# Performance work log

Measured on AMD Instinct MI355X. Metric: run time of the kernel, lower is better.

## Reference

```python
import jax, jax.numpy as jnp
import numpy as np

# dims: n=batch, T=n_shifts, dX=16, dU=8, H=256 hidden, L=128 ldim, K=64 n_aux (L=2K)

def setup_inputs() -> dict:
    key = jax.random.key(0)
    ks = jax.random.split(key, 16)
    n, T, dX, dU, H, L, K = 64, 64, 16, 8, 256, 128, 64
    def lin(k, fan_in, shape):
        return (jax.random.uniform(k, shape, jnp.float32) * 2.0 - 1.0) / np.sqrt(fan_in)
    xs = jax.random.normal(ks[0], (n, T, dX), jnp.float32)
    us = jax.random.normal(ks[1], (n, T - 1, dU), jnp.float32)
    theta = jax.random.uniform(ks[2], (K,), jnp.float32) * (2.0 * np.pi)
    inp = {
        'xs': xs, 'us': us,
        # stacked x-aux encoders (K copies): BN affine, 3 linear layers (last no bias), output scale
        'x_gamma': jnp.ones((K, dX)), 'x_beta': jnp.zeros((K, dX)),
        'xW1': lin(ks[3], dX, (K, dX, H)), 'xb1': jnp.zeros((K, H)),
        'xW2': lin(ks[4], H, (K, H, H)), 'xb2': jnp.zeros((K, H)),
        'xW3': lin(ks[5], H, (K, H, L)), 'x_scale': jnp.ones((K, L)),
        # stacked u-aux encoders (K copies)
        'u_gamma': jnp.ones((K, dU)), 'u_beta': jnp.zeros((K, dU)),
        'uW1': lin(ks[6], dU, (K, dU, H)), 'ub1': jnp.zeros((K, H)),
        'uW2': lin(ks[7], H, (K, H, H)), 'ub2': jnp.zeros((K, H)),
        'uW3': lin(ks[8], H, (K, H, L)), 'u_scale': jnp.ones((K, L)),
        # Jordan-block complex eigenvalues (|lam| ~ 0.95)
        'reL': 0.95 * jnp.cos(theta), 'imL': 0.95 * jnp.sin(theta),
        # decoder C: Linear(ldim, dim, bias=False) -> weight [dX, L]
        'C_W': lin(ks[9], L, (dX, L)),
    }
    return inp


def _encoder(x, gamma, beta, W1, b1, W2, b2, W3, scale):
    # x: [M, D]; stacked params over K nets. BN stats (training mode) are per-feature over M,
    # identical across nets since the same x feeds every net.
    mu = x.mean(0)
    var = ((x - mu) ** 2).mean(0)
    xn = (x - mu) * jax.lax.rsqrt(var + 1e-5)          # [M, D]
    h = xn[None] * gamma[:, None, :] + beta[:, None, :]  # [K, M, D]
    h = jax.nn.leaky_relu(jnp.einsum('kmd,kdh->kmh', h, W1) + b1[:, None, :])
    h = jax.nn.leaky_relu(jnp.einsum('kmd,kdh->kmh', h, W2) + b2[:, None, :])
    h = jnp.einsum('kmd,kdh->kmh', h, W3)               # last layer: no bias
    return h * scale[:, None, :]                        # [K, M, L]


def reference(xs, us, x_gamma, x_beta, xW1, xb1, xW2, xb2, xW3, x_scale,
              u_gamma, u_beta, uW1, ub1, uW2, ub2, uW3, u_scale, reL, imL, C_W):
    n, T, dX = xs.shape
    K = reL.shape[0]
    L = 2 * K
    Tm1 = T - 1
    # phi1s: [n, T, K(net), K(pair), 2]
    phi = _encoder(xs.reshape(n * T, dX), x_gamma, x_beta, xW1, xb1, xW2, xb2, xW3, x_scale)
    phi1s = jnp.moveaxis(phi, 0, 1).reshape(n, T, K, K, 2)
    # ures = psi(u) - psi(0): [n, T-1, K, K, 2]
    uflat = us.reshape(n * Tm1, -1)
    psi_u = _encoder(uflat, u_gamma, u_beta, uW1, ub1, uW2, ub2, uW3, u_scale)
    psi_0 = _encoder(jnp.zeros_like(uflat), u_gamma, u_beta, uW1, ub1, uW2, ub2, uW3, u_scale)
    ures = jnp.moveaxis(psi_u - psi_0, 0, 1).reshape(n, Tm1, K, K, 2)
    # block-diagonal Koopman: per net j a 2x2 rotation-scale [[re, im], [-im, re]]
    R = jnp.stack([jnp.stack([reL, imL], -1), jnp.stack([-imL, reL], -1)], -2)  # [K, 2, 2]

    def step(p, u_t):
        p = jnp.einsum('bjkc,jcd->bjkd', p + u_t, R)
        return p, p

    _, preds = jax.lax.scan(step, phi1s[:, 0], jnp.moveaxis(ures, 0, 1))
    preds = jnp.moveaxis(preds, 0, 1)  # [n, T-1, K, K, 2]

    def phi2y(p):
        # sum over net axis (-3), flatten pair dims -> [.., L], decode with C
        return p.sum(-3).reshape(*p.shape[:-3], L) @ C_W.T

    y = phi2y(phi1s[:, 1:])
    y_pred = phi2y(preds)
    return y, y_pred
```

## Files before the change

kernel.cpp:

```cpp
#include <hip/hip_runtime.h>

typedef __bf16 bf16_t;
typedef __bf16 bf16x8 __attribute__((ext_vector_type(8)));
typedef __bf16 bf16x4 __attribute__((ext_vector_type(4)));
typedef float  f32x4  __attribute__((ext_vector_type(4)));

#define PHI_JS  (4096 * 128 + 64)
#define PSIU_JS (4032 * 128 + 64)

__global__ __launch_bounds__(256) void prep_all_kernel(
    const float* __restrict__ xW1, const float* __restrict__ xb1,
    const float* __restrict__ xg,  const float* __restrict__ xbeta,
    const float* __restrict__ uW1, const float* __restrict__ ub1,
    const float* __restrict__ ug,  const float* __restrict__ ubeta,
    const float* __restrict__ xW2, const float* __restrict__ uW2,
    const float* __restrict__ xW3, const float* __restrict__ uW3,
    const float* __restrict__ x_scale, const float* __restrict__ u_scale,
    const float* __restrict__ ub2,
    const float* __restrict__ xs, const float* __restrict__ us,
    bf16_t* __restrict__ xW1t, float* __restrict__ xb1p,
    bf16_t* __restrict__ uW1t, float* __restrict__ ub1p,
    bf16_t* __restrict__ xW2t, bf16_t* __restrict__ uW2t,
    bf16_t* __restrict__ xW3t, bf16_t* __restrict__ uW3t,
    float* __restrict__ psi0, float* __restrict__ part)
{
    const int t = blockIdx.x, tid = threadIdx.x;
    __shared__ float tile[32][33];
    __shared__ float h1[256], h2[256];

    if (t < 12288) {
        const float* in; bf16_t* outp; const float* scale = nullptr;
        int j, r0, c0, C;
        if (t < 8192) {
            C = 256;
            j = (t & 4095) >> 6;
            const int tl = t & 63; r0 = (tl >> 3) * 32; c0 = (tl & 7) * 32;
            if (t < 4096) { in = xW2; outp = xW2t; }
            else          { in = uW2; outp = uW2t; }
        } else {
            C = 128;
            const int l = t - 8192;
            j = (l & 2047) >> 5;
            const int tl = l & 31; r0 = (tl >> 2) * 32; c0 = (tl & 3) * 32;
            if (l < 2048) { in = xW3; outp = xW3t; scale = x_scale + j * 128; }
            else          { in = uW3; outp = uW3t; scale = u_scale + j * 128; }
        }
        const int R = 256;
        in   += (size_t)j * R * C;
        bf16_t* op = outp + (size_t)j * R * C;
        const int tx = tid & 31, ty = tid >> 5;
        #pragma unroll
        for (int i = 0; i < 4; i++)
            tile[ty + i * 8][tx] = in[(size_t)(r0 + ty + i * 8) * C + c0 + tx];
        __syncthreads();
        #pragma unroll
        for (int i = 0; i < 4; i++) {
            int c = c0 + ty + i * 8;
            float sc = scale ? scale[c] : 1.f;
            op[(size_t)c * R + r0 + tx] = (bf16_t)(tile[tx][ty + i * 8] * sc);
        }
    } else if (t < 12416) {
        const int bid = t - 12288, j = bid & 63, h = tid;
        const float *W1, *b1, *gamma, *beta; bf16_t* W1t; float* b1p; int D;
        if (bid < 64) { W1 = xW1; b1 = xb1; gamma = xg; beta = xbeta; W1t = xW1t; b1p = xb1p; D = 16; }
        else          { W1 = uW1; b1 = ub1; gamma = ug; beta = ubeta; W1t = uW1t; b1p = ub1p; D = 8; }
        float bacc = b1[j * 256 + h];
        bf16_t* orow = W1t + (size_t)(j * 256 + h) * 32;
        for (int d = 0; d < 32; d++) orow[d] = (bf16_t)0.f;
        for (int d = 0; d < D; d++) {
            float w = W1[((size_t)j * D + d) * 256 + h];
            orow[d] = (bf16_t)(gamma[j * D + d] * w);
            bacc += beta[j * D + d] * w;
        }
        b1p[j * 256 + h] = bacc;
    } else if (t < 12480) {
        const int j = t - 12416, h = tid;
        {
            float bacc = ub1[j * 256 + h];
            #pragma unroll
            for (int d = 0; d < 8; d++)
                bacc += ubeta[j * 8 + d] * uW1[((size_t)j * 8 + d) * 256 + h];
            h1[h] = fmaxf(bacc, 0.01f * bacc);
        }
        __syncthreads();
        {
            float acc = ub2[j * 256 + h];
            const float* w2 = uW2 + (size_t)j * 65536 + h;
            #pragma unroll 8
            for (int d = 0; d < 256; d++) acc += h1[d] * w2[d * 256];
            h2[h] = fmaxf(acc, 0.01f * acc);
        }
        __syncthreads();
        if (h < 128) {
            float acc = 0.f;
            const float* w3 = uW3 + (size_t)j * 32768 + h;
            #pragma unroll 8
            for (int d = 0; d < 256; d++) acc += h2[d] * w3[d * 128];
            psi0[j * 128 + h] = acc * u_scale[j * 128 + h];
        }
    } else {
        const int bid = t - 12480;
        const bool isx = bid < 64;
        const float* x = isx ? xs : us;
        const int D   = isx ? 16 : 8;
        const int lb  = isx ? bid : bid - 64;
        const int per = isx ? 1024 : 1008;
        const int start = lb * per;
        float a = 0.f, b = 0.f;
        for (int idx = start + tid; idx < start + per; idx += 256) {
            float v = x[idx];
            a += v; b += v * v;
        }
        float* s1 = h1; float* s2 = h2;
        s1[tid] = a; s2[tid] = b;
        __syncthreads();
        if (tid < D) {
            float sa = 0.f, sb = 0.f;
            for (int k = tid; k < 256; k += D) { sa += s1[k]; sb += s2[k]; }
            part[bid * 32 + tid]      = sa;
            part[bid * 32 + 16 + tid] = sb;
        }
    }
}

__global__ __launch_bounds__(512, 4) void fused_mlp_kernel(
    const float* __restrict__ xs, const float* __restrict__ us,
    const float* __restrict__ part,
    const bf16_t* __restrict__ xW1t, const float* __restrict__ xb1p,
    const bf16_t* __restrict__ xW2t, const float* __restrict__ xb2,
    const bf16_t* __restrict__ xW3t,
    const bf16_t* __restrict__ uW1t, const float* __restrict__ ub1p,
    const bf16_t* __restrict__ uW2t, const float* __restrict__ ub2,
    const bf16_t* __restrict__ uW3t,
    bf16_t* __restrict__ phi, bf16_t* __restrict__ psiu)
{
    const int bid  = blockIdx.x;
    const int xcd  = bid & 7;
    const int slot = bid >> 3;
    const int band = slot >> 6;
    const int t64  = slot & 63;
    const int j    = xcd * 8 + band;
    const bool is_x = t64 < 32;
    const int tile  = is_x ? t64 : (t64 - 32);

    const float*  In  = is_x ? xs   : us;
    const int     D   = is_x ? 16   : 8;
    const bf16_t* W1t = is_x ? xW1t : uW1t;
    const float*  b1p = is_x ? xb1p : ub1p;
    const bf16_t* W2t = is_x ? xW2t : uW2t;
    const float*  b2  = is_x ? xb2  : ub2;
    const bf16_t* W3t = is_x ? xW3t : uW3t;
    bf16_t* outp      = is_x ? phi  : psiu;
    const int M       = is_x ? 4096 : 4032;
    const size_t JS   = is_x ? (size_t)PHI_JS : (size_t)PSIU_JS;

    const int row0 = tile * 128;
    const int tid  = threadIdx.x;
    const int wave = tid >> 6;
    const int lane = tid & 63;
    const int quad = lane >> 4;
    const int l16  = lane & 15;
    const int lo2  = l16 & 3, hi2 = l16 >> 2;

    __shared__ __align__(16) bf16_t hs[128 * 256];
    __shared__ float stats_s[32];

    if (tid < 16) {
        if (is_x) {
            float sa = 0.f, sb = 0.f;
            #pragma unroll 8
            for (int b = 0; b < 64; b++) { sa += part[b * 32 + tid]; sb += part[b * 32 + 16 + tid]; }
            float mu = sa / 4096.f, var = sb / 4096.f - mu * mu;
            stats_s[tid] = mu; stats_s[16 + tid] = rsqrtf(var + 1e-5f);
        } else if (tid < 8) {
            float sa = 0.f, sb = 0.f;
            #pragma unroll 8
            for (int b = 64; b < 96; b++) { sa += part[b * 32 + tid]; sb += part[b * 32 + 16 + tid]; }
            float mu = sa / 4032.f, var = sb / 4032.f - mu * mu;
            stats_s[tid] = mu; stats_s[16 + tid] = rsqrtf(var + 1e-5f);
        }
    }
    __syncthreads();

    const f32x4 vzero = {0.f, 0.f, 0.f, 0.f};

    char* const hsB = (char*)hs;
    const char* const abase = hsB + l16 * 512 + ((quad ^ lo2) << 4);
    const int  wlow0 = (quad >> 1) ^ lo2;
    char* const wbase = hsB + l16 * 512 + ((wave ^ hi2) << 6) + ((quad & 1) << 3);

    {
        bf16x8 wfr[2];
        #pragma unroll
        for (int nbi = 0; nbi < 2; nbi++)
            wfr[nbi] = *reinterpret_cast<const bf16x8*>(
                W1t + (size_t)(j * 256 + wave * 32 + nbi * 16 + l16) * 32 + quad * 8);

        f32x4 acc[8][2];
        #pragma unroll
        for (int a = 0; a < 8; a++) { acc[a][0] = vzero; acc[a][1] = vzero; }

        const int c0 = quad * 8;
        #pragma unroll
        for (int mb = 0; mb < 8; mb++) {
            bf16x8 a;
            if (c0 < D) {
                int row = row0 + mb * 16 + l16;
                if (row > M - 1) row = M - 1;
                const float* xp = In + (size_t)row * D + c0;
                f32x4 v0 = *reinterpret_cast<const f32x4*>(xp);
                f32x4 v1 = *reinterpret_cast<const f32x4*>(xp + 4);
                #pragma unroll
                for (int e = 0; e < 4; e++) a[e]     = (bf16_t)((v0[e] - stats_s[c0 + e])     * stats_s[16 + c0 + e]);
                #pragma unroll
                for (int e = 0; e < 4; e++) a[4 + e] = (bf16_t)((v1[e] - stats_s[c0 + 4 + e]) * stats_s[16 + c0 + 4 + e]);
            } else {
                #pragma unroll
                for (int e = 0; e < 8; e++) a[e] = (bf16_t)0.f;
            }
            #pragma unroll
            for (int nbi = 0; nbi < 2; nbi++)
                acc[mb][nbi] = __builtin_amdgcn_mfma_f32_16x16x32_bf16(
                    wfr[nbi], a, acc[mb][nbi], 0, 0, 0);
        }

        #pragma unroll
        for (int nbi = 0; nbi < 2; nbi++) {
            const f32x4 bias = *reinterpret_cast<const f32x4*>(
                b1p + j * 256 + wave * 32 + nbi * 16 + quad * 4);
            char* wp = wbase + ((wlow0 ^ (nbi << 1)) << 4);
            #pragma unroll
            for (int mb = 0; mb < 8; mb++) {
                bf16x4 pk;
                #pragma unroll
                for (int r = 0; r < 4; r++) {
                    float v = acc[mb][nbi][r] + bias[r];
                    v = fmaxf(v, 0.01f * v);
                    pk[r] = (bf16_t)v;
                }
                *reinterpret_cast<bf16x4*>(wp + mb * 8192) = pk;
            }
        }
    }
    __syncthreads();

    {
        f32x4 acc[8][2];
        #pragma unroll
        for (int a = 0; a < 8; a++) { acc[a][0] = vzero; acc[a][1] = vzero; }

        const bf16_t* w2base = W2t + ((size_t)j * 256 + wave * 32 + l16) * 256 + quad * 8;

        bf16x8 wr[3][2];
        #pragma unroll
        for (int d = 0; d < 3; d++)
            #pragma unroll
            for (int nbi = 0; nbi < 2; nbi++)
                wr[d][nbi] = *reinterpret_cast<const bf16x8*>(w2base + nbi * 4096 + d * 32);

        #pragma unroll
        for (int kk = 0; kk < 8; kk++) {
            const int c = kk % 3;
            const char* ap = abase + ((kk ^ hi2) << 6);
            bf16x8 av0[4];
            #pragma unroll
            for (int mb = 0; mb < 4; mb++)
                av0[mb] = *reinterpret_cast<const bf16x8*>(ap + mb * 8192);
            #pragma unroll
            for (int nbi = 0; nbi < 2; nbi++)
                #pragma unroll
                for (int mb = 0; mb < 4; mb++)
                    acc[mb][nbi] = __builtin_amdgcn_mfma_f32_16x16x32_bf16(
                        wr[c][nbi], av0[mb], acc[mb][nbi], 0, 0, 0);
            bf16x8 av1[4];
            #pragma unroll
            for (int mb = 0; mb < 4; mb++)
                av1[mb] = *reinterpret_cast<const bf16x8*>(ap + (mb + 4) * 8192);
            #pragma unroll
            for (int nbi = 0; nbi < 2; nbi++)
                #pragma unroll
                for (int mb = 4; mb < 8; mb++)
                    acc[mb][nbi] = __builtin_amdgcn_mfma_f32_16x16x32_bf16(
                        wr[c][nbi], av1[mb - 4], acc[mb][nbi], 0, 0, 0);
            if (kk < 5) {
                #pragma unroll
                for (int nbi = 0; nbi < 2; nbi++)
                    wr[c][nbi] = *reinterpret_cast<const bf16x8*>(
                        w2base + nbi * 4096 + (kk + 3) * 32);
            }
        }
        __syncthreads();
        #pragma unroll
        for (int nbi = 0; nbi < 2; nbi++) {
            const f32x4 bias = *reinterpret_cast<const f32x4*>(
                b2 + j * 256 + wave * 32 + nbi * 16 + quad * 4);
            char* wp = wbase + ((wlow0 ^ (nbi << 1)) << 4);
            #pragma unroll
            for (int mb = 0; mb < 8; mb++) {
                bf16x4 pk;
                #pragma unroll
                for (int r = 0; r < 4; r++) {
                    float v = acc[mb][nbi][r] + bias[r];
                    v = fmaxf(v, 0.01f * v);
                    pk[r] = (bf16_t)v;
                }
                *reinterpret_cast<bf16x4*>(wp + mb * 8192) = pk;
            }
        }
    }
    __syncthreads();

    {
        f32x4 acc[8];
        #pragma unroll
        for (int a = 0; a < 8; a++) acc[a] = vzero;

        const bf16_t* w3base = W3t + ((size_t)j * 128 + wave * 16 + l16) * 256 + quad * 8;

        bf16x8 wr[3];
        #pragma unroll
        for (int d = 0; d < 3; d++)
            wr[d] = *reinterpret_cast<const bf16x8*>(w3base + d * 32);

        #pragma unroll
        for (int kk = 0; kk < 8; kk++) {
            const int c = kk % 3;
            const char* ap = abase + ((kk ^ hi2) << 6);
            bf16x8 av0[4];
            #pragma unroll
            for (int mb = 0; mb < 4; mb++)
                av0[mb] = *reinterpret_cast<const bf16x8*>(ap + mb * 8192);
            #pragma unroll
            for (int mb = 0; mb < 4; mb++)
                acc[mb] = __builtin_amdgcn_mfma_f32_16x16x32_bf16(
                    wr[c], av0[mb], acc[mb], 0, 0, 0);
            bf16x8 av1[4];
            #pragma unroll
            for (int mb = 0; mb < 4; mb++)
                av1[mb] = *reinterpret_cast<const bf16x8*>(ap + (mb + 4) * 8192);
            #pragma unroll
            for (int mb = 4; mb < 8; mb++)
                acc[mb] = __builtin_amdgcn_mfma_f32_16x16x32_bf16(
                    wr[c], av1[mb - 4], acc[mb], 0, 0, 0);
            if (kk < 5)
                wr[c] = *reinterpret_cast<const bf16x8*>(w3base + (kk + 3) * 32);
        }
        __syncthreads();
        {
            const int sp3 = (wave * 2 + (quad >> 1)) ^ l16;
            char* w3p = hsB + l16 * 256 + sp3 * 16 + ((quad & 1) << 3);
            #pragma unroll
            for (int mb = 0; mb < 8; mb++) {
                bf16x4 pk;
                #pragma unroll
                for (int r = 0; r < 4; r++) pk[r] = (bf16_t)acc[mb][r];
                *reinterpret_cast<bf16x4*>(w3p + mb * 4096) = pk;
            }
        }
    }
    __syncthreads();
    #pragma unroll
    for (int p = 0; p < 4; p++) {
        const int rr = p * 32 + (tid >> 4);
        const int s  = tid & 15;
        if (row0 + rr < M) {
            bf16x8 v = *reinterpret_cast<const bf16x8*>(hs + rr * 128 + (s ^ (rr & 15)) * 8);
            *reinterpret_cast<bf16x8*>(outp + (size_t)j * JS + (size_t)(row0 + rr) * 128 + s * 8) = v;
        }
    }
}

__global__ __launch_bounds__(256) void scan_kernel(
    const bf16_t* __restrict__ phi, const bf16_t* __restrict__ psiu,
    const float* __restrict__ psi0, const float* __restrict__ reL,
    const float* __restrict__ imL, float* __restrict__ scratchP,
    float* __restrict__ scratchY) {
    const int b = blockIdx.x >> 3, jg = blockIdx.x & 7;
    const int tid = threadIdx.x;
    const int wave = tid >> 6, lane = tid & 63;
    __shared__ float redP[2][4][128];
    __shared__ float redY[2][4][128];

    const int j0 = jg * 8 + wave * 2;
    float sx0, sy0, sx1, sy1;
    float p0x0, p0y0, p0x1, p0y1, lre0, lim0, lre1, lim1;
    {
        unsigned v0 = *reinterpret_cast<const unsigned*>(
            phi + (size_t)j0 * PHI_JS + (size_t)(b * 64) * 128 + lane * 2);
        unsigned v1 = *reinterpret_cast<const unsigned*>(
            phi + (size_t)(j0 + 1) * PHI_JS + (size_t)(b * 64) * 128 + lane * 2);
        sx0 = __uint_as_float(v0 << 16); sy0 = __uint_as_float(v0 & 0xFFFF0000u);
        sx1 = __uint_as_float(v1 << 16); sy1 = __uint_as_float(v1 & 0xFFFF0000u);
        float2 p0 = *reinterpret_cast<const float2*>(psi0 + j0 * 128 + lane * 2);
        float2 p1 = *reinterpret_cast<const float2*>(psi0 + (j0 + 1) * 128 + lane * 2);
        p0x0 = p0.x; p0y0 = p0.y; p0x1 = p1.x; p0y1 = p1.y;
        lre0 = reL[j0]; lim0 = imL[j0]; lre1 = reL[j0 + 1]; lim1 = imL[j0 + 1];
    }
    const bf16_t* up0 = psiu + (size_t)j0 * PSIU_JS + (size_t)(b * 63) * 128 + lane * 2;
    const bf16_t* up1 = psiu + (size_t)(j0 + 1) * PSIU_JS + (size_t)(b * 63) * 128 + lane * 2;
    const bf16_t* pp0 = phi + (size_t)j0 * PHI_JS + (size_t)(b * 64 + 1) * 128 + lane * 2;
    const bf16_t* pp1 = phi + (size_t)(j0 + 1) * PHI_JS + (size_t)(b * 64 + 1) * 128 + lane * 2;
    unsigned cur0 = *reinterpret_cast<const unsigned*>(up0);
    unsigned cur1 = *reinterpret_cast<const unsigned*>(up1);
    unsigned curp0 = *reinterpret_cast<const unsigned*>(pp0);
    unsigned curp1 = *reinterpret_cast<const unsigned*>(pp1);
    float* outP = scratchP + (size_t)blockIdx.x * 63 * 128;
    float* outY = scratchY + (size_t)blockIdx.x * 63 * 128;

    for (int t = 0; t < 63; t++) {
        unsigned nx0 = 0, nx1 = 0, np0 = 0, np1 = 0;
        if (t < 62) {
            nx0 = *reinterpret_cast<const unsigned*>(up0 + (t + 1) * 128);
            nx1 = *reinterpret_cast<const unsigned*>(up1 + (t + 1) * 128);
            np0 = *reinterpret_cast<const unsigned*>(pp0 + (t + 1) * 128);
            np1 = *reinterpret_cast<const unsigned*>(pp1 + (t + 1) * 128);
        }
        float px = sx0 + (__uint_as_float(cur0 << 16) - p0x0);
        float py = sy0 + (__uint_as_float(cur0 & 0xFFFF0000u) - p0y0);
        sx0 = px * lre0 - py * lim0;
        sy0 = px * lim0 + py * lre0;
        px = sx1 + (__uint_as_float(cur1 << 16) - p0x1);
        py = sy1 + (__uint_as_float(cur1 & 0xFFFF0000u) - p0y1);
        sx1 = px * lre1 - py * lim1;
        sy1 = px * lim1 + py * lre1;
        float yx = __uint_as_float(curp0 << 16) + __uint_as_float(curp1 << 16);
        float yy = __uint_as_float(curp0 & 0xFFFF0000u) + __uint_as_float(curp1 & 0xFFFF0000u);
        const int db = t & 1;
        redP[db][wave][lane * 2]     = sx0 + sx1;
        redP[db][wave][lane * 2 + 1] = sy0 + sy1;
        redY[db][wave][lane * 2]     = yx;
        redY[db][wave][lane * 2 + 1] = yy;
        __syncthreads();
        if (tid < 128)
            outP[t * 128 + tid] = redP[db][0][tid] + redP[db][1][tid]
                                + redP[db][2][tid] + redP[db][3][tid];
        else {
            const int tl = tid - 128;
            outY[t * 128 + tl] = redY[db][0][tl] + redY[db][1][tl]
                               + redY[db][2][tl] + redY[db][3][tl];
        }
        cur0 = nx0; cur1 = nx1; curp0 = np0; curp1 = np1;
    }
}

__global__ __launch_bounds__(256) void decode_kernel(
    const float* __restrict__ scratchP, const float* __restrict__ scratchY,
    const float* __restrict__ C_W,
    float* __restrict__ y, float* __restrict__ ypred) {
    const int tg = threadIdx.x >> 6;
    const int l  = threadIdx.x & 63;
    const int t  = blockIdx.x * 4 + tg;
    const int b  = blockIdx.y;
    __shared__ float SP[4][128];
    __shared__ float SY[4][128];
    if (t < 63) {
        float s0 = 0.f, s1 = 0.f, u0 = 0.f, u1 = 0.f;
        #pragma unroll
        for (int jg = 0; jg < 8; jg++) {
            const size_t base = ((size_t)(b * 8 + jg) * 63 + t) * 128 + l * 2;
            float2 vp = *reinterpret_cast<const float2*>(scratchP + base);
            float2 vy = *reinterpret_cast<const float2*>(scratchY + base);
            s0 += vp.x; s1 += vp.y;
            u0 += vy.x; u1 += vy.y;
        }
        SP[tg][l * 2] = s0; SP[tg][l * 2 + 1] = s1;
        SY[tg][l * 2] = u0; SY[tg][l * 2 + 1] = u1;
        const int o = l >> 2, q = l & 3;
        float accP = 0.f, accY = 0.f;
        #pragma unroll
        for (int i = 0; i < 32; i++) {
            const float c = C_W[o * 128 + q * 32 + i];
            accP += SP[tg][q * 32 + i] * c;
            accY += SY[tg][q * 32 + i] * c;
        }
        accP += __shfl_xor(accP, 2, 4);
        accP += __shfl_xor(accP, 1, 4);
        accY += __shfl_xor(accY, 2, 4);
        accY += __shfl_xor(accY, 1, 4);
        if (q == 0) {
            ypred[(b * 63 + t) * 16 + o] = accP;
            y[(b * 63 + t) * 16 + o]     = accY;
        }
    }
}

extern "C" void kernel_launch(void* const* d_in, const int* in_sizes, int n_in,
                              void* d_out, int out_size, void* d_ws, size_t ws_size,
                              hipStream_t stream) {
    const float* xs      = (const float*)d_in[0];
    const float* us      = (const float*)d_in[1];
    const float* x_gamma = (const float*)d_in[2];
    const float* x_beta  = (const float*)d_in[3];
    const float* xW1     = (const float*)d_in[4];
    const float* xb1     = (const float*)d_in[5];
    const float* xW2     = (const float*)d_in[6];
    const float* xb2     = (const float*)d_in[7];
    const float* xW3     = (const float*)d_in[8];
    const float* x_scale = (const float*)d_in[9];
    const float* u_gamma = (const float*)d_in[10];
    const float* u_beta  = (const float*)d_in[11];
    const float* uW1     = (const float*)d_in[12];
    const float* ub1     = (const float*)d_in[13];
    const float* uW2     = (const float*)d_in[14];
    const float* ub2     = (const float*)d_in[15];
    const float* uW3     = (const float*)d_in[16];
    const float* u_scale = (const float*)d_in[17];
    const float* reL     = (const float*)d_in[18];
    const float* imL     = (const float*)d_in[19];
    const float* C_W     = (const float*)d_in[20];

    char* ws = (char*)d_ws;
    size_t off = 0;
    auto alloc = [&](size_t bytes) -> char* {
        char* p = ws + off;
        off += (bytes + 255) & ~(size_t)255;
        return p;
    };
    float*  part = (float*)alloc(96 * 32 * 4);
    bf16_t* xW1t = (bf16_t*)alloc((size_t)64 * 256 * 32 * 2);
    float*  xb1p = (float*) alloc((size_t)64 * 256 * 4);
    bf16_t* xW2t = (bf16_t*)alloc((size_t)64 * 256 * 256 * 2);
    bf16_t* xW3t = (bf16_t*)alloc((size_t)64 * 128 * 256 * 2);
    bf16_t* uW1t = (bf16_t*)alloc((size_t)64 * 256 * 32 * 2);
    float*  ub1p = (float*) alloc((size_t)64 * 256 * 4);
    bf16_t* uW2t = (bf16_t*)alloc((size_t)64 * 256 * 256 * 2);
    bf16_t* uW3t = (bf16_t*)alloc((size_t)64 * 128 * 256 * 2);
    float*  psi0 = (float*) alloc((size_t)64 * 128 * 4);
    bf16_t* phi  = (bf16_t*)alloc((size_t)64 * PHI_JS  * 2);
    bf16_t* psiu = (bf16_t*)alloc((size_t)64 * PSIU_JS * 2);
    float*  scrP = (float*) alloc((size_t)512 * 63 * 128 * 4);
    float*  scrY = (float*) alloc((size_t)512 * 63 * 128 * 4);

    float* y_out     = (float*)d_out;
    float* ypred_out = y_out + 64 * 63 * 16;

    prep_all_kernel<<<12576, 256, 0, stream>>>(
        xW1, xb1, x_gamma, x_beta, uW1, ub1, u_gamma, u_beta,
        xW2, uW2, xW3, uW3, x_scale, u_scale, ub2, xs, us,
        xW1t, xb1p, uW1t, ub1p, xW2t, uW2t, xW3t, uW3t, psi0, part);
    fused_mlp_kernel<<<4096, 512, 0, stream>>>(
        xs, us, part,
        xW1t, xb1p, xW2t, xb2, xW3t, uW1t, ub1p, uW2t, ub2, uW3t, phi, psiu);
    scan_kernel<<<512, 256, 0, stream>>>(phi, psiu, psi0, reL, imL, scrP, scrY);
    decode_kernel<<<dim3(16, 64), 256, 0, stream>>>(scrP, scrY, C_W, y_out, ypred_out);
}
```

Baseline: 355.7 us.

## Fuse decode into scan via atomics and move psi0 MLP into fused kernel

```diff
diff --git a/kernel.cpp b/kernel.cpp
--- a/kernel.cpp
+++ b/kernel.cpp
@@ -16,13 +16,12 @@
     const float* __restrict__ xW2, const float* __restrict__ uW2,
     const float* __restrict__ xW3, const float* __restrict__ uW3,
     const float* __restrict__ x_scale, const float* __restrict__ u_scale,
-    const float* __restrict__ ub2,
     const float* __restrict__ xs, const float* __restrict__ us,
     bf16_t* __restrict__ xW1t, float* __restrict__ xb1p,
     bf16_t* __restrict__ uW1t, float* __restrict__ ub1p,
     bf16_t* __restrict__ xW2t, bf16_t* __restrict__ uW2t,
     bf16_t* __restrict__ xW3t, bf16_t* __restrict__ uW3t,
-    float* __restrict__ psi0, float* __restrict__ part)
+    float* __restrict__ part, float* __restrict__ zout)
 {
     const int t = blockIdx.x, tid = threadIdx.x;
     __shared__ float tile[32][33];
@@ -73,33 +72,8 @@
             bacc += beta[j * D + d] * w;
         }
         b1p[j * 256 + h] = bacc;
-    } else if (t < 12480) {
-        const int j = t - 12416, h = tid;
-        {
-            float bacc = ub1[j * 256 + h];
-            #pragma unroll
-            for (int d = 0; d < 8; d++)
-                bacc += ubeta[j * 8 + d] * uW1[((size_t)j * 8 + d) * 256 + h];
-            h1[h] = fmaxf(bacc, 0.01f * bacc);
-        }
-        __syncthreads();
-        {
-            float acc = ub2[j * 256 + h];
-            const float* w2 = uW2 + (size_t)j * 65536 + h;
-            #pragma unroll 8
-            for (int d = 0; d < 256; d++) acc += h1[d] * w2[d * 256];
-            h2[h] = fmaxf(acc, 0.01f * acc);
-        }
-        __syncthreads();
-        if (h < 128) {
-            float acc = 0.f;
-            const float* w3 = uW3 + (size_t)j * 32768 + h;
-            #pragma unroll 8
-            for (int d = 0; d < 256; d++) acc += h2[d] * w3[d * 128];
-            psi0[j * 128 + h] = acc * u_scale[j * 128 + h];
-        }
-    } else {
-        const int bid = t - 12480;
+    } else if (t < 12512) {
+        const int bid = t - 12416;
         const bool isx = bid < 64;
         const float* x = isx ? xs : us;
         const int D   = isx ? 16 : 8;
@@ -120,6 +94,10 @@
             part[bid * 32 + tid]      = sa;
             part[bid * 32 + 16 + tid] = sb;
         }
+    } else {
+        const int g = (t - 12512) * 256 + tid;
+        for (int i = g; i < 2 * 64 * 63 * 16; i += 64 * 256)
+            zout[i] = 0.f;
     }
 }
 
@@ -132,9 +110,62 @@
     const bf16_t* __restrict__ uW1t, const float* __restrict__ ub1p,
     const bf16_t* __restrict__ uW2t, const float* __restrict__ ub2,
     const bf16_t* __restrict__ uW3t,
+    const float* __restrict__ uW1r, const float* __restrict__ ub1r,
+    const float* __restrict__ ubetar, const float* __restrict__ uW2r,
+    const float* __restrict__ uW3r, const float* __restrict__ u_scaler,
+    float* __restrict__ psi0_out,
     bf16_t* __restrict__ phi, bf16_t* __restrict__ psiu)
 {
     const int bid  = blockIdx.x;
+    const int tid  = threadIdx.x;
+
+    __shared__ __align__(16) bf16_t hs[128 * 256];
+    __shared__ float stats_s[32];
+
+    if (bid >= 4096) {
+        const int j = bid - 4096;
+        float* fb  = (float*)hs;
+        float* h1  = fb;
+        float* h2  = fb + 256;
+        float* tmp = fb + 512;
+        const int h = tid & 255, half = tid >> 8;
+        if (half == 0) {
+            float bacc = ub1r[j * 256 + h];
+            #pragma unroll
+            for (int d = 0; d < 8; d++)
+                bacc += ubetar[j * 8 + d] * uW1r[((size_t)j * 8 + d) * 256 + h];
+            h1[h] = fmaxf(bacc, 0.01f * bacc);
+        }
+        __syncthreads();
+        {
+            float acc = (half == 0) ? ub2[j * 256 + h] : 0.f;
+            const float* w2 = uW2r + (size_t)j * 65536 + (size_t)half * 128 * 256 + h;
+            #pragma unroll 16
+            for (int d = 0; d < 128; d++) acc += h1[half * 128 + d] * w2[(size_t)d * 256];
+            tmp[tid] = acc;
+        }
+        __syncthreads();
+        if (half == 0) {
+            float v = tmp[h] + tmp[h + 256];
+            h2[h] = fmaxf(v, 0.01f * v);
+        }
+        __syncthreads();
+        {
+            const int h3 = tid & 127, qd = tid >> 7;
+            float acc = 0.f;
+            const float* w3 = uW3r + (size_t)j * 32768 + (size_t)qd * 64 * 128 + h3;
+            #pragma unroll 16
+            for (int d = 0; d < 64; d++) acc += h2[qd * 64 + d] * w3[(size_t)d * 128];
+            tmp[tid] = acc;
+        }
+        __syncthreads();
+        if (tid < 128)
+            psi0_out[j * 128 + tid] =
+                (tmp[tid] + tmp[tid + 128] + tmp[tid + 256] + tmp[tid + 384])
+                * u_scaler[j * 128 + tid];
+        return;
+    }
+
     const int xcd  = bid & 7;
     const int slot = bid >> 3;
     const int band = slot >> 6;
@@ -155,15 +186,11 @@
     const size_t JS   = is_x ? (size_t)PHI_JS : (size_t)PSIU_JS;
 
     const int row0 = tile * 128;
-    const int tid  = threadIdx.x;
     const int wave = tid >> 6;
     const int lane = tid & 63;
     const int quad = lane >> 4;
     const int l16  = lane & 15;
     const int lo2  = l16 & 3, hi2 = l16 >> 2;
-
-    __shared__ __align__(16) bf16_t hs[128 * 256];
-    __shared__ float stats_s[32];
 
     if (tid < 16) {
         if (is_x) {
@@ -373,13 +400,17 @@
 __global__ __launch_bounds__(256) void scan_kernel(
     const bf16_t* __restrict__ phi, const bf16_t* __restrict__ psiu,
     const float* __restrict__ psi0, const float* __restrict__ reL,
-    const float* __restrict__ imL, float* __restrict__ scratchP,
-    float* __restrict__ scratchY) {
+    const float* __restrict__ imL, const float* __restrict__ C_W,
+    float* __restrict__ y, float* __restrict__ ypred) {
     const int b = blockIdx.x >> 3, jg = blockIdx.x & 7;
     const int tid = threadIdx.x;
     const int wave = tid >> 6, lane = tid & 63;
     __shared__ float redP[2][4][128];
     __shared__ float redY[2][4][128];
+    __shared__ float SP[128], SY[128];
+    __shared__ float Cs[2048];
+    #pragma unroll
+    for (int i = 0; i < 8; i++) Cs[tid + i * 256] = C_W[tid + i * 256];
 
     const int j0 = jg * 8 + wave * 2;
     float sx0, sy0, sx1, sy1;
@@ -404,8 +435,8 @@
     unsigned cur1 = *reinterpret_cast<const unsigned*>(up1);
     unsigned curp0 = *reinterpret_cast<const unsigned*>(pp0);
     unsigned curp1 = *reinterpret_cast<const unsigned*>(pp1);
-    float* outP = scratchP + (size_t)blockIdx.x * 63 * 128;
-    float* outY = scratchY + (size_t)blockIdx.x * 63 * 128;
+
+    const int oo = (tid & 127) >> 3, qq = tid & 7;
 
     for (int t = 0; t < 63; t++) {
         unsigned nx0 = 0, nx1 = 0, np0 = 0, np1 = 0;
@@ -432,55 +463,30 @@
         redY[db][wave][lane * 2 + 1] = yy;
         __syncthreads();
         if (tid < 128)
-            outP[t * 128 + tid] = redP[db][0][tid] + redP[db][1][tid]
-                                + redP[db][2][tid] + redP[db][3][tid];
+            SP[tid] = redP[db][0][tid] + redP[db][1][tid]
+                    + redP[db][2][tid] + redP[db][3][tid];
         else {
             const int tl = tid - 128;
-            outY[t * 128 + tl] = redY[db][0][tl] + redY[db][1][tl]
-                               + redY[db][2][tl] + redY[db][3][tl];
+            SY[tl] = redY[db][0][tl] + redY[db][1][tl]
+                   + redY[db][2][tl] + redY[db][3][tl];
+        }
+        __syncthreads();
+        {
+            const float* S = (tid < 128) ? SP : SY;
+            float acc = 0.f;
+            #pragma unroll
+            for (int i = 0; i < 16; i++)
+                acc += S[qq * 16 + i] * Cs[oo * 128 + qq * 16 + i];
+            acc += __shfl_xor(acc, 4, 8);
+            acc += __shfl_xor(acc, 2, 8);
+            acc += __shfl_xor(acc, 1, 8);
+            if (qq == 0) {
+                float* dst = (tid < 128) ? (ypred + (b * 63 + t) * 16 + oo)
+                                         : (y     + (b * 63 + t) * 16 + oo);
+                atomicAdd(dst, acc);
+            }
         }
         cur0 = nx0; cur1 = nx1; curp0 = np0; curp1 = np1;
-    }
-}
-
-__global__ __launch_bounds__(256) void decode_kernel(
-    const float* __restrict__ scratchP, const float* __restrict__ scratchY,
-    const float* __restrict__ C_W,
-    float* __restrict__ y, float* __restrict__ ypred) {
-    const int tg = threadIdx.x >> 6;
-    const int l  = threadIdx.x & 63;
-    const int t  = blockIdx.x * 4 + tg;
-    const int b  = blockIdx.y;
-    __shared__ float SP[4][128];
-    __shared__ float SY[4][128];
-    if (t < 63) {
-        float s0 = 0.f, s1 = 0.f, u0 = 0.f, u1 = 0.f;
-        #pragma unroll
-        for (int jg = 0; jg < 8; jg++) {
-            const size_t base = ((size_t)(b * 8 + jg) * 63 + t) * 128 + l * 2;
-            float2 vp = *reinterpret_cast<const float2*>(scratchP + base);
-            float2 vy = *reinterpret_cast<const float2*>(scratchY + base);
-            s0 += vp.x; s1 += vp.y;
-            u0 += vy.x; u1 += vy.y;
-        }
-        SP[tg][l * 2] = s0; SP[tg][l * 2 + 1] = s1;
-        SY[tg][l * 2] = u0; SY[tg][l * 2 + 1] = u1;
-        const int o = l >> 2, q = l & 3;
-        float accP = 0.f, accY = 0.f;
-        #pragma unroll
-        for (int i = 0; i < 32; i++) {
-            const float c = C_W[o * 128 + q * 32 + i];
-            accP += SP[tg][q * 32 + i] * c;
-            accY += SY[tg][q * 32 + i] * c;
-        }
-        accP += __shfl_xor(accP, 2, 4);
-        accP += __shfl_xor(accP, 1, 4);
-        accY += __shfl_xor(accY, 2, 4);
-        accY += __shfl_xor(accY, 1, 4);
-        if (q == 0) {
-            ypred[(b * 63 + t) * 16 + o] = accP;
-            y[(b * 63 + t) * 16 + o]     = accY;
-        }
     }
 }
 
@@ -528,19 +534,19 @@
     float*  psi0 = (float*) alloc((size_t)64 * 128 * 4);
     bf16_t* phi  = (bf16_t*)alloc((size_t)64 * PHI_JS  * 2);
     bf16_t* psiu = (bf16_t*)alloc((size_t)64 * PSIU_JS * 2);
-    float*  scrP = (float*) alloc((size_t)512 * 63 * 128 * 4);
-    float*  scrY = (float*) alloc((size_t)512 * 63 * 128 * 4);
 
     float* y_out     = (float*)d_out;
     float* ypred_out = y_out + 64 * 63 * 16;
 
     prep_all_kernel<<<12576, 256, 0, stream>>>(
         xW1, xb1, x_gamma, x_beta, uW1, ub1, u_gamma, u_beta,
-        xW2, uW2, xW3, uW3, x_scale, u_scale, ub2, xs, us,
-        xW1t, xb1p, uW1t, ub1p, xW2t, uW2t, xW3t, uW3t, psi0, part);
-    fused_mlp_kernel<<<4096, 512, 0, stream>>>(
+        xW2, uW2, xW3, uW3, x_scale, u_scale, xs, us,
+        xW1t, xb1p, uW1t, ub1p, xW2t, uW2t, xW3t, uW3t, part, y_out);
+    fused_mlp_kernel<<<4160, 512, 0, stream>>>(
         xs, us, part,
-        xW1t, xb1p, xW2t, xb2, xW3t, uW1t, ub1p, uW2t, ub2, uW3t, phi, psiu);
-    scan_kernel<<<512, 256, 0, stream>>>(phi, psiu, psi0, reL, imL, scrP, scrY);
-    decode_kernel<<<dim3(16, 64), 256, 0, stream>>>(scrP, scrY, C_W, y_out, ypred_out);
+        xW1t, xb1p, xW2t, xb2, xW3t, uW1t, ub1p, uW2t, ub2, uW3t,
+        uW1, ub1, u_beta, uW2, uW3, u_scale, psi0,
+        phi, psiu);
+    scan_kernel<<<512, 256, 0, stream>>>(
+        phi, psiu, psi0, reL, imL, C_W, y_out, ypred_out);
 }
```

Result: no change. 357.2 us (+0.4%).
